# Kernel tuning notes

Measured on AMD Instinct MI355X. Metric: run time of the kernel, lower is better.

Reference implementation:

```python
import jax, jax.numpy as jnp
import numpy as np

N, E, IN, C, H = 50000, 1600000, 128, 64, 2
HC = H * C  # 128; num_out = 128, conv_out channels per head = 64
NEG_SLOPE = 0.2


def setup_inputs() -> dict:
    key = jax.random.key(0)
    ks = jax.random.split(key, 16)
    x = jax.random.normal(ks[0], (N, IN), dtype=jnp.float32)
    edge_index = jax.random.randint(ks[1], (2, E), 0, N, dtype=jnp.int64)

    def gat_params(k, fan_in, heads, out_ch):
        k1, k2, k3 = jax.random.split(k, 3)
        sc = 1.0 / np.sqrt(fan_in)
        W = jax.random.normal(k1, (fan_in, heads * out_ch), dtype=jnp.float32) * sc
        a_src = jax.random.normal(k2, (heads, out_ch), dtype=jnp.float32) * 0.1
        a_dst = jax.random.normal(k3, (heads, out_ch), dtype=jnp.float32) * 0.1
        b = jnp.zeros((heads * out_ch,), dtype=jnp.float32)
        return W, a_src, a_dst, b

    W_in, a_src_in, a_dst_in, b_in = gat_params(ks[2], IN, H, C)
    # 2 hidden layers, stacked on leading axis
    Wh, ash, adh, bh = [], [], [], []
    for i in range(2):
        W, a_s, a_d, b = gat_params(ks[3 + i], HC, H, C)
        Wh.append(W); ash.append(a_s); adh.append(a_d); bh.append(b)
    W_h = jnp.stack(Wh); a_src_h = jnp.stack(ash)
    a_dst_h = jnp.stack(adh); b_h = jnp.stack(bh)
    W_out, a_src_out, a_dst_out, b_out = gat_params(ks[6], HC, H, C)
    return dict(x=x, edge_index=edge_index,
                W_in=W_in, a_src_in=a_src_in, a_dst_in=a_dst_in, b_in=b_in,
                W_h=W_h, a_src_h=a_src_h, a_dst_h=a_dst_h, b_h=b_h,
                W_out=W_out, a_src_out=a_src_out, a_dst_out=a_dst_out, b_out=b_out)


def gat_layer(xf, src, dst, W, a_src, a_dst, b, heads, out_ch):
    n = xf.shape[0]
    h = (xf @ W).reshape(n, heads, out_ch)              # [N,H,C]
    e_src = jnp.einsum('nhc,hc->nh', h, a_src)          # [N,H]
    e_dst = jnp.einsum('nhc,hc->nh', h, a_dst)
    e = jax.nn.leaky_relu(e_src[src] + e_dst[dst], NEG_SLOPE)  # [E',H]
    m = jax.ops.segment_max(e, dst, num_segments=n)     # softmax over edges per dst
    p = jnp.exp(e - m[dst])
    s = jax.ops.segment_sum(p, dst, num_segments=n)
    alpha = p / (s[dst] + 1e-16)
    out = jax.ops.segment_sum(alpha[:, :, None] * h[src], dst, num_segments=n)
    return out.reshape(n, heads * out_ch) + b


def reference(x, edge_index, W_in, a_src_in, a_dst_in, b_in,
              W_h, a_src_h, a_dst_h, b_h,
              W_out, a_src_out, a_dst_out, b_out):
    # add self loops (PyG GATConv default add_self_loops=True)
    loops = jnp.arange(N, dtype=edge_index.dtype)
    src = jnp.concatenate([edge_index[0], loops])
    dst = jnp.concatenate([edge_index[1], loops])

    h = jax.nn.relu(gat_layer(x, src, dst, W_in, a_src_in, a_dst_in, b_in, H, C))
    for i in range(2):
        h = jax.nn.relu(gat_layer(h, src, dst, W_h[i], a_src_h[i], a_dst_h[i], b_h[i], H, C))
    out = gat_layer(h, src, dst, W_out, a_src_out, a_dst_out, b_out, H, C)
    return out
```

## Files before the change

### kernel.cpp

```cpp
#include <hip/hip_runtime.h>

#define NNODES 50000
#define NEDGES 1600000
#define NEG_SLOPE 0.2f

#define SCAN_NB 256
#define SCAN_CH 196

#define MT_ROWS 64
#define NMT 782
#define GEMM_BLOCKS 768

typedef __attribute__((ext_vector_type(8))) short short8;
typedef __attribute__((ext_vector_type(4))) float f32x4;
typedef __attribute__((ext_vector_type(4))) unsigned short us4;

static __device__ __forceinline__ unsigned short f2bf(float f) {
    unsigned u = __float_as_uint(f);
    unsigned r = u + 0x7FFFu + ((u >> 16) & 1u);
    return (unsigned short)(r >> 16);
}
static __device__ __forceinline__ float bf2f(unsigned short h) {
    return __uint_as_float(((unsigned)h) << 16);
}
static __device__ __forceinline__ unsigned short f2h(float f) {
    union { _Float16 x; unsigned short u; } c;
    c.x = (_Float16)f;
    return c.u;
}
static __device__ __forceinline__ float h2f(unsigned short u) {
    union { unsigned short u; _Float16 x; } c;
    c.u = u;
    return (float)c.x;
}


__global__ void k_count(const int* __restrict__ ei, int* __restrict__ count,
                        int* __restrict__ pos) {
    int t = blockIdx.x * blockDim.x + threadIdx.x;
    int stride = gridDim.x * blockDim.x;
    #pragma unroll
    for (int i = 0; i < 8; i++) {
        int e = t + i * stride;
        if (e < NEDGES) pos[e] = atomicAdd(&count[ei[NEDGES + e]], 1);
    }
}

__global__ __launch_bounds__(256) void k_bsum(const int* __restrict__ count,
                                              int* __restrict__ bsum) {
    __shared__ int red[4];
    int t = threadIdx.x, b = blockIdx.x;
    int idx = b * SCAN_CH + t;
    int v = (t < SCAN_CH && idx < NNODES) ? count[idx] + 1 : 0;
    #pragma unroll
    for (int m = 1; m <= 32; m <<= 1) v += __shfl_xor(v, m);
    if ((t & 63) == 0) red[t >> 6] = v;
    __syncthreads();
    if (t == 0) bsum[b] = red[0] + red[1] + red[2] + red[3];
}

__global__ __launch_bounds__(256) void k_bscan(const int* __restrict__ bsum,
                                               int* __restrict__ boff,
                                               int* __restrict__ row_ptr) {
    __shared__ int s[256];
    int t = threadIdx.x;
    int v = bsum[t];
    s[t] = v;
    __syncthreads();
    for (int off = 1; off < 256; off <<= 1) {
        int u = (t >= off) ? s[t - off] : 0;
        __syncthreads();
        s[t] += u;
        __syncthreads();
    }
    boff[t] = s[t] - v;
    if (t == 255) row_ptr[NNODES] = s[255];
}

__global__ __launch_bounds__(256) void k_rowptr(const int* __restrict__ count,
                                                const int* __restrict__ boff,
                                                int* __restrict__ row_ptr,
                                                int* __restrict__ csr_src) {
    __shared__ int s[256];
    int t = threadIdx.x, b = blockIdx.x;
    int idx = b * SCAN_CH + t;
    bool valid = (t < SCAN_CH && idx < NNODES);
    int v = valid ? count[idx] + 1 : 0;
    s[t] = v;
    __syncthreads();
    for (int off = 1; off < 256; off <<= 1) {
        int u = (t >= off) ? s[t - off] : 0;
        __syncthreads();
        s[t] += u;
        __syncthreads();
    }
    if (valid) {
        int run = boff[b] + s[t] - v;
        row_ptr[idx] = run;
        csr_src[run] = idx;
    }
}

__global__ void k_scatter(const int* __restrict__ ei, const int* __restrict__ row_ptr,
                          const int* __restrict__ pos, int* __restrict__ csr_src) {
    int t = blockIdx.x * blockDim.x + threadIdx.x;
    int stride = gridDim.x * blockDim.x;
    #pragma unroll
    for (int i = 0; i < 4; i++) {
        int e = t + i * stride;
        if (e < NEDGES) {
            int s = ei[e];
            int d = ei[NEDGES + e];
            __builtin_nontemporal_store(s, &csr_src[row_ptr[d] + 1 + pos[e]]);
        }
    }
}

__global__ __launch_bounds__(256) void k_wprep(const float* __restrict__ W0,
                                               const float* __restrict__ Wh,
                                               const float* __restrict__ Wout,
                                               unsigned short* __restrict__ wthi,
                                               unsigned short* __restrict__ wtlo) {
    int t = blockIdx.x * blockDim.x + threadIdx.x;
    int l = t >> 14;
    int i = t & 16383;
    int k = i >> 7, n = i & 127;
    const float* src = (l == 0) ? W0 : (l == 3) ? Wout : (Wh + (size_t)(l - 1) * 16384);
    float v = src[i];
    unsigned short h = f2bf(v);
    wthi[(size_t)l * 16384 + n * 128 + k] = h;
    wtlo[(size_t)l * 16384 + n * 128 + k] = f2bf(v - bf2f(h));
}

__global__ __launch_bounds__(256, 3) void k_gemm_mfma(
        const float* __restrict__ X,
        const unsigned short* __restrict__ Ahi, const unsigned short* __restrict__ Alo,
        const unsigned short* __restrict__ Wthi, const unsigned short* __restrict__ Wtlo,
        const float* __restrict__ a_src, const float* __restrict__ a_dst,
        unsigned short* __restrict__ Hh,
        float* __restrict__ e_src, float* __restrict__ e_dst, int use_x)
{
    __shared__ __align__(16) short sAhi[MT_ROWS * 128];
    __shared__ __align__(16) short sAlo[MT_ROWS * 128];
    __shared__ float eS[4][MT_ROWS];
    __shared__ float eD[4][MT_ROWS];

    const int tid  = threadIdx.x;
    const int lane = tid & 63;
    const int w    = tid >> 6;
    const int l15  = lane & 15;
    const int quad = lane >> 4;

    short8 Bh[2][4], Bl[2][4];
    #pragma unroll
    for (int nt = 0; nt < 2; nt++) {
        int n = w * 32 + nt * 16 + l15;
        #pragma unroll
        for (int ks = 0; ks < 4; ks++) {
            Bh[nt][ks] = *(const short8*)(Wthi + (size_t)n * 128 + ks * 32 + quad * 8);
            Bl[nt][ks] = *(const short8*)(Wtlo + (size_t)n * 128 + ks * 32 + quad * 8);
        }
    }
    float as0 = a_src[w * 32 + l15],      ad0 = a_dst[w * 32 + l15];
    float as1 = a_src[w * 32 + 16 + l15], ad1 = a_dst[w * 32 + 16 + l15];

    for (int mt0 = blockIdx.x; mt0 < NMT; mt0 += GEMM_BLOCKS) {
        const int row0 = mt0 * MT_ROWS;

        for (int i = tid; i < MT_ROWS * 16; i += 256) {
            int m  = i >> 4;
            int kc = i & 15;
            int g  = row0 + m; if (g > NNODES - 1) g = NNODES - 1;
            int cp = kc ^ (m & 15);
            short8 vh, vl;
            if (use_x) {
                float4 xa = *(const float4*)(X + (size_t)g * 128 + kc * 8);
                float4 xb = *(const float4*)(X + (size_t)g * 128 + kc * 8 + 4);
                float xs[8] = {xa.x, xa.y, xa.z, xa.w, xb.x, xb.y, xb.z, xb.w};
                #pragma unroll
                for (int q = 0; q < 8; q++) {
                    unsigned short h = f2bf(xs[q]);
                    vh[q] = (short)h;
                    vl[q] = (short)f2bf(xs[q] - bf2f(h));
                }
            } else {
                vh = *(const short8*)(Ahi + (size_t)g * 128 + kc * 8);
                vl = *(const short8*)(Alo + (size_t)g * 128 + kc * 8);
            }
            *(short8*)&sAhi[m * 128 + cp * 8] = vh;
            *(short8*)&sAlo[m * 128 + cp * 8] = vl;
        }
        __syncthreads();

        f32x4 zero = {0.f, 0.f, 0.f, 0.f};
        f32x4 acc[4][2];
        #pragma unroll
        for (int mt = 0; mt < 4; mt++) { acc[mt][0] = zero; acc[mt][1] = zero; }
        #pragma unroll
        for (int mt = 0; mt < 4; mt++) {
            int m = mt * 16 + l15;
            #pragma unroll
            for (int ks = 0; ks < 4; ks++) {
                int kc = ks * 4 + quad;
                int cp = kc ^ l15;
                short8 ah = *(const short8*)&sAhi[m * 128 + cp * 8];
                short8 al = *(const short8*)&sAlo[m * 128 + cp * 8];
                #pragma unroll
                for (int nt = 0; nt < 2; nt++) {
                    acc[mt][nt] = __builtin_amdgcn_mfma_f32_16x16x32_bf16(ah, Bh[nt][ks], acc[mt][nt], 0, 0, 0);
                    acc[mt][nt] = __builtin_amdgcn_mfma_f32_16x16x32_bf16(al, Bh[nt][ks], acc[mt][nt], 0, 0, 0);
                    acc[mt][nt] = __builtin_amdgcn_mfma_f32_16x16x32_bf16(ah, Bl[nt][ks], acc[mt][nt], 0, 0, 0);
                }
            }
        }

        #pragma unroll
        for (int mt = 0; mt < 4; mt++) {
            #pragma unroll
            for (int r = 0; r < 4; r++) {
                int m = mt * 16 + quad * 4 + r;
                int g = row0 + m;
                float v0 = acc[mt][0][r], v1 = acc[mt][1][r];
                if (g < NNODES) {
                    int n0 = w * 32 + l15;
                    Hh[(size_t)g * 128 + n0]      = f2h(v0);
                    Hh[(size_t)g * 128 + n0 + 16] = f2h(v1);
                }
                float ps = v0 * as0 + v1 * as1;
                float pd = v0 * ad0 + v1 * ad1;
                ps += __shfl_xor(ps, 1); ps += __shfl_xor(ps, 2);
                ps += __shfl_xor(ps, 4); ps += __shfl_xor(ps, 8);
                pd += __shfl_xor(pd, 1); pd += __shfl_xor(pd, 2);
                pd += __shfl_xor(pd, 4); pd += __shfl_xor(pd, 8);
                if (l15 == 0) { eS[w][m] = ps; eD[w][m] = pd; }
            }
        }
        __syncthreads();
        if (tid < MT_ROWS * 2) {
            int m = tid >> 1, head = tid & 1;
            int g = row0 + m;
            if (g < NNODES) {
                e_src[g * 2 + head] = eS[head * 2][m] + eS[head * 2 + 1][m];
                e_dst[g * 2 + head] = eD[head * 2][m] + eD[head * 2 + 1][m];
            }
        }
        __syncthreads();
    }
}

__global__ __launch_bounds__(256) void k_aggregate_h(const unsigned short* __restrict__ Hh,
                                                     const float* __restrict__ e_src,
                                                     const float* __restrict__ e_dst,
                                                     const int* __restrict__ row_ptr,
                                                     const int* __restrict__ csr_src,
                                                     const float* __restrict__ bias,
                                                     unsigned short* __restrict__ ohi,
                                                     unsigned short* __restrict__ olo) {
    int lane = threadIdx.x & 63;
    int wv   = threadIdx.x >> 6;
    int d    = blockIdx.x * 4 + wv;
    if (d >= NNODES) return;
    int half = lane >> 5;
    int li   = lane & 31;
    int head = li >> 4;
    int c0   = li * 4;
    float ed = e_dst[d * 2 + head];
    int beg = row_ptr[d], end = row_ptr[d + 1];
    f32x4 acc = {0.f, 0.f, 0.f, 0.f};
    float ssum = 0.f;
    int j = beg;
    for (; j + 16 <= end; j += 16) {
        int s[8];
        #pragma unroll
        for (int u = 0; u < 8; u++) s[u] = csr_src[j + 2 * u + half];
        us4 q[8];
        #pragma unroll
        for (int u = 0; u < 8; u++) q[u] = *(const us4*)(Hh + (size_t)s[u] * 128 + c0);
        float p[8];
        #pragma unroll
        for (int u = 0; u < 8; u++) {
            float t = e_src[s[u] * 2 + head] + ed;
            t = t > 0.f ? t : NEG_SLOPE * t;
            p[u] = __expf(t);
        }
        #pragma unroll
        for (int u = 0; u < 8; u++) {
            acc[0] += p[u] * h2f(q[u][0]);
            acc[1] += p[u] * h2f(q[u][1]);
            acc[2] += p[u] * h2f(q[u][2]);
            acc[3] += p[u] * h2f(q[u][3]);
            ssum   += p[u];
        }
    }
    for (; j < end; j += 2) {
        int idx = j + half;
        bool valid = idx < end;
        int s = csr_src[valid ? idx : end - 1];
        float t = e_src[s * 2 + head] + ed;
        t = t > 0.f ? t : NEG_SLOPE * t;
        float p = valid ? __expf(t) : 0.f;
        us4 q = *(const us4*)(Hh + (size_t)s * 128 + c0);
        acc[0] += p * h2f(q[0]);
        acc[1] += p * h2f(q[1]);
        acc[2] += p * h2f(q[2]);
        acc[3] += p * h2f(q[3]);
        ssum   += p;
    }
    acc[0] += __shfl_xor(acc[0], 32);
    acc[1] += __shfl_xor(acc[1], 32);
    acc[2] += __shfl_xor(acc[2], 32);
    acc[3] += __shfl_xor(acc[3], 32);
    ssum   += __shfl_xor(ssum,   32);
    if (half == 0) {
        float inv = 1.0f / ssum;
        float4 bv = *(const float4*)(bias + c0);
        float o0 = fmaxf(acc[0] * inv + bv.x, 0.f);
        float o1 = fmaxf(acc[1] * inv + bv.y, 0.f);
        float o2 = fmaxf(acc[2] * inv + bv.z, 0.f);
        float o3 = fmaxf(acc[3] * inv + bv.w, 0.f);
        unsigned short h0 = f2bf(o0), h1 = f2bf(o1), h2 = f2bf(o2), h3 = f2bf(o3);
        *(ushort4*)&ohi[(size_t)d * 128 + c0] = make_ushort4(h0, h1, h2, h3);
        *(ushort4*)&olo[(size_t)d * 128 + c0] =
            make_ushort4(f2bf(o0 - bf2f(h0)), f2bf(o1 - bf2f(h1)),
                         f2bf(o2 - bf2f(h2)), f2bf(o3 - bf2f(h3)));
    }
}

__global__ __launch_bounds__(256) void k_aggregate_f(const unsigned short* __restrict__ Hh,
                                                     const float* __restrict__ e_src,
                                                     const float* __restrict__ e_dst,
                                                     const int* __restrict__ row_ptr,
                                                     const int* __restrict__ csr_src,
                                                     const float* __restrict__ bias,
                                                     float* __restrict__ outf) {
    int lane = threadIdx.x & 63;
    int wv   = threadIdx.x >> 6;
    int d    = blockIdx.x * 4 + wv;
    if (d >= NNODES) return;
    int half = lane >> 5;
    int li   = lane & 31;
    int head = li >> 4;
    int c0   = li * 4;
    float ed = e_dst[d * 2 + head];
    int beg = row_ptr[d], end = row_ptr[d + 1];
    f32x4 acc = {0.f, 0.f, 0.f, 0.f};
    float ssum = 0.f;
    int j = beg;
    for (; j + 16 <= end; j += 16) {
        int s[8];
        #pragma unroll
        for (int u = 0; u < 8; u++) s[u] = csr_src[j + 2 * u + half];
        us4 q[8];
        #pragma unroll
        for (int u = 0; u < 8; u++) q[u] = *(const us4*)(Hh + (size_t)s[u] * 128 + c0);
        float p[8];
        #pragma unroll
        for (int u = 0; u < 8; u++) {
            float t = e_src[s[u] * 2 + head] + ed;
            t = t > 0.f ? t : NEG_SLOPE * t;
            p[u] = __expf(t);
        }
        #pragma unroll
        for (int u = 0; u < 8; u++) {
            acc[0] += p[u] * h2f(q[u][0]);
            acc[1] += p[u] * h2f(q[u][1]);
            acc[2] += p[u] * h2f(q[u][2]);
            acc[3] += p[u] * h2f(q[u][3]);
            ssum   += p[u];
        }
    }
    for (; j < end; j += 2) {
        int idx = j + half;
        bool valid = idx < end;
        int s = csr_src[valid ? idx : end - 1];
        float t = e_src[s * 2 + head] + ed;
        t = t > 0.f ? t : NEG_SLOPE * t;
        float p = valid ? __expf(t) : 0.f;
        us4 q = *(const us4*)(Hh + (size_t)s * 128 + c0);
        acc[0] += p * h2f(q[0]);
        acc[1] += p * h2f(q[1]);
        acc[2] += p * h2f(q[2]);
        acc[3] += p * h2f(q[3]);
        ssum   += p;
    }
    acc[0] += __shfl_xor(acc[0], 32);
    acc[1] += __shfl_xor(acc[1], 32);
    acc[2] += __shfl_xor(acc[2], 32);
    acc[3] += __shfl_xor(acc[3], 32);
    ssum   += __shfl_xor(ssum,   32);
    if (half == 0) {
        float inv = 1.0f / ssum;
        float4 bv = *(const float4*)(bias + c0);
        *(float4*)(outf + (size_t)d * 128 + c0) =
            make_float4(acc[0] * inv + bv.x, acc[1] * inv + bv.y,
                        acc[2] * inv + bv.z, acc[3] * inv + bv.w);
    }
}


extern "C" void kernel_launch(void* const* d_in, const int* in_sizes, int n_in,
                              void* d_out, int out_size, void* d_ws, size_t ws_size,
                              hipStream_t stream) {
    const float* x  = (const float*)d_in[0];
    const int*   ei = (const int*)d_in[1];

    char* ws = (char*)d_ws;
    size_t off = 0;
    auto alloc = [&](size_t bytes) {
        void* p = ws + off;
        off = (off + bytes + 255) & ~(size_t)255;
        return p;
    };
    int*            count   = (int*)alloc((size_t)NNODES * 4);
    int*            row_ptr = (int*)alloc((size_t)(NNODES + 1) * 4);
    int*            csr     = (int*)alloc((size_t)(NEDGES + NNODES) * 4);
    int*            pos     = (int*)alloc((size_t)NEDGES * 4);
    int*            bsum    = (int*)alloc((size_t)SCAN_NB * 4);
    int*            boff    = (int*)alloc((size_t)SCAN_NB * 4);
    unsigned short* hh      = (unsigned short*)alloc((size_t)NNODES * 128 * 2);
    unsigned short* wthi    = (unsigned short*)alloc((size_t)4 * 16384 * 2);
    unsigned short* wtlo    = (unsigned short*)alloc((size_t)4 * 16384 * 2);
    float*          es      = (float*)alloc((size_t)NNODES * 2 * 4);
    float*          edv     = (float*)alloc((size_t)NNODES * 2 * 4);
    (void)ws_size; (void)in_sizes; (void)n_in; (void)out_size;

    unsigned short* hi = (unsigned short*)d_out;
    unsigned short* lo = hi + (size_t)NNODES * 128;

    const float* W0   = (const float*)d_in[2];
    const float* W_h  = (const float*)d_in[6];
    const float* Wout = (const float*)d_in[10];

    hipMemsetAsync(count, 0, (size_t)NNODES * 4, stream);
    k_count  <<<(NEDGES + 8 * 256 - 1) / (8 * 256), 256, 0, stream>>>(ei, count, pos);
    k_wprep  <<<256, 256, 0, stream>>>(W0, W_h, Wout, wthi, wtlo);
    k_bsum   <<<SCAN_NB, 256, 0, stream>>>(count, bsum);
    k_bscan  <<<1, 256, 0, stream>>>(bsum, boff, row_ptr);
    k_rowptr <<<SCAN_NB, 256, 0, stream>>>(count, boff, row_ptr, csr);
    k_scatter<<<(NEDGES + 4 * 256 - 1) / (4 * 256), 256, 0, stream>>>(ei, row_ptr, pos, csr);

    const float* ash = (const float*)d_in[7];
    const float* adh = (const float*)d_in[8];
    const float* bh  = (const float*)d_in[9];

    struct Layer { const float *as, *ad, *b; };
    Layer L[4] = {
        { (const float*)d_in[3],  (const float*)d_in[4],  (const float*)d_in[5]  },
        { ash,        adh,        bh        },
        { ash + 128,  adh + 128,  bh + 128  },
        { (const float*)d_in[11], (const float*)d_in[12], (const float*)d_in[13] },
    };

    const int agg_blocks = (NNODES + 3) / 4;
    for (int l = 0; l < 4; l++) {
        k_gemm_mfma<<<GEMM_BLOCKS, 256, 0, stream>>>(
            x, hi, lo, wthi + (size_t)l * 16384, wtlo + (size_t)l * 16384,
            L[l].as, L[l].ad, hh, es, edv, l == 0 ? 1 : 0);
        if (l < 3) {
            k_aggregate_h<<<agg_blocks, 256, 0, stream>>>(hh, es, edv, row_ptr, csr,
                                                          L[l].b, hi, lo);
        } else {
            k_aggregate_f<<<agg_blocks, 256, 0, stream>>>(hh, es, edv, row_ptr, csr,
                                                          L[l].b, (float*)d_out);
        }
    }
}
```

Before: 597.2 us.

## Fuse edge counting into first GEMM launch and widen aggregation gathers to 8 halves

Result: faster. 537.6 us (-10.0%).

```diff
diff --git a/kernel.cpp b/kernel.cpp
--- a/kernel.cpp
+++ b/kernel.cpp
@@ -10,10 +10,12 @@
 #define MT_ROWS 64
 #define NMT 782
 #define GEMM_BLOCKS 768
+#define COUNT_BLOCKS 256
 
 typedef __attribute__((ext_vector_type(8))) short short8;
 typedef __attribute__((ext_vector_type(4))) float f32x4;
-typedef __attribute__((ext_vector_type(4))) unsigned short us4;
+typedef __attribute__((ext_vector_type(8))) _Float16 h16x8;
+typedef __attribute__((ext_vector_type(8))) unsigned short us8;
 
 static __device__ __forceinline__ unsigned short f2bf(float f) {
     unsigned u = __float_as_uint(f);
@@ -28,23 +30,7 @@
     c.x = (_Float16)f;
     return c.u;
 }
-static __device__ __forceinline__ float h2f(unsigned short u) {
-    union { unsigned short u; _Float16 x; } c;
-    c.u = u;
-    return (float)c.x;
-}
-
-
-__global__ void k_count(const int* __restrict__ ei, int* __restrict__ count,
-                        int* __restrict__ pos) {
-    int t = blockIdx.x * blockDim.x + threadIdx.x;
-    int stride = gridDim.x * blockDim.x;
-    #pragma unroll
-    for (int i = 0; i < 8; i++) {
-        int e = t + i * stride;
-        if (e < NEDGES) pos[e] = atomicAdd(&count[ei[NEDGES + e]], 1);
-    }
-}
+
 
 __global__ __launch_bounds__(256) void k_bsum(const int* __restrict__ count,
                                               int* __restrict__ bsum) {
@@ -138,12 +124,25 @@
         const unsigned short* __restrict__ Wthi, const unsigned short* __restrict__ Wtlo,
         const float* __restrict__ a_src, const float* __restrict__ a_dst,
         unsigned short* __restrict__ Hh,
-        float* __restrict__ e_src, float* __restrict__ e_dst, int use_x)
+        float* __restrict__ e_src, float* __restrict__ e_dst, int use_x,
+        const int* __restrict__ ei, int* __restrict__ count, int* __restrict__ pos)
 {
     __shared__ __align__(16) short sAhi[MT_ROWS * 128];
     __shared__ __align__(16) short sAlo[MT_ROWS * 128];
     __shared__ float eS[4][MT_ROWS];
     __shared__ float eD[4][MT_ROWS];
+
+    if (blockIdx.x >= GEMM_BLOCKS) {
+        int t = (blockIdx.x - GEMM_BLOCKS) * 256 + threadIdx.x;
+        for (int base = t; base < NEDGES; base += 8 * 65536) {
+            #pragma unroll
+            for (int i = 0; i < 8; i++) {
+                int e = base + i * 65536;
+                if (e < NEDGES) pos[e] = atomicAdd(&count[ei[NEDGES + e]], 1);
+            }
+        }
+        return;
+    }
 
     const int tid  = threadIdx.x;
     const int lane = tid & 63;
@@ -248,6 +247,96 @@
     }
 }
 
+template <int FINAL>
+__device__ __forceinline__ void agg_body(const _Float16* __restrict__ Hh,
+                                         const float* __restrict__ e_src,
+                                         const float* __restrict__ e_dst,
+                                         const int* __restrict__ row_ptr,
+                                         const int* __restrict__ csr_src,
+                                         const float* __restrict__ bias,
+                                         float* __restrict__ outf,
+                                         unsigned short* __restrict__ ohi,
+                                         unsigned short* __restrict__ olo) {
+    int lane = threadIdx.x & 63;
+    int wv   = threadIdx.x >> 6;
+    int d    = blockIdx.x * 4 + wv;
+    if (d >= NNODES) return;
+    int qt   = lane >> 4;
+    int cl   = lane & 15;
+    int head = cl >> 3;
+    int c0   = cl * 8;
+    float ed = e_dst[d * 2 + head];
+    int beg = row_ptr[d], end = row_ptr[d + 1];
+    float acc[8] = {0.f, 0.f, 0.f, 0.f, 0.f, 0.f, 0.f, 0.f};
+    float ssum = 0.f;
+    int j = beg;
+    for (; j + 16 <= end; j += 16) {
+        int s0 = csr_src[j + qt],      s1 = csr_src[j + 4 + qt];
+        int s2 = csr_src[j + 8 + qt],  s3 = csr_src[j + 12 + qt];
+        h16x8 h0 = *(const h16x8*)(Hh + (size_t)s0 * 128 + c0);
+        h16x8 h1 = *(const h16x8*)(Hh + (size_t)s1 * 128 + c0);
+        h16x8 h2 = *(const h16x8*)(Hh + (size_t)s2 * 128 + c0);
+        h16x8 h3 = *(const h16x8*)(Hh + (size_t)s3 * 128 + c0);
+        float t0 = e_src[s0 * 2 + head] + ed, t1 = e_src[s1 * 2 + head] + ed;
+        float t2 = e_src[s2 * 2 + head] + ed, t3 = e_src[s3 * 2 + head] + ed;
+        t0 = t0 > 0.f ? t0 : NEG_SLOPE * t0;  t1 = t1 > 0.f ? t1 : NEG_SLOPE * t1;
+        t2 = t2 > 0.f ? t2 : NEG_SLOPE * t2;  t3 = t3 > 0.f ? t3 : NEG_SLOPE * t3;
+        float p0 = __expf(t0), p1 = __expf(t1), p2 = __expf(t2), p3 = __expf(t3);
+        #pragma unroll
+        for (int c = 0; c < 8; c++)
+            acc[c] += p0 * (float)h0[c] + p1 * (float)h1[c]
+                    + p2 * (float)h2[c] + p3 * (float)h3[c];
+        ssum += p0 + p1 + p2 + p3;
+    }
+    for (; j < end; j += 4) {
+        int idx = j + qt;
+        bool valid = idx < end;
+        int s = csr_src[valid ? idx : end - 1];
+        float t = e_src[s * 2 + head] + ed;
+        t = t > 0.f ? t : NEG_SLOPE * t;
+        float p = valid ? __expf(t) : 0.f;
+        h16x8 hq = *(const h16x8*)(Hh + (size_t)s * 128 + c0);
+        #pragma unroll
+        for (int c = 0; c < 8; c++) acc[c] += p * (float)hq[c];
+        ssum += p;
+    }
+    #pragma unroll
+    for (int c = 0; c < 8; c++) {
+        acc[c] += __shfl_xor(acc[c], 16);
+        acc[c] += __shfl_xor(acc[c], 32);
+    }
+    ssum += __shfl_xor(ssum, 16);
+    ssum += __shfl_xor(ssum, 32);
+    if (qt == 0) {
+        float inv = 1.0f / ssum;
+        f32x4 b0 = *(const f32x4*)(bias + c0);
+        f32x4 b1 = *(const f32x4*)(bias + c0 + 4);
+        float o[8];
+        #pragma unroll
+        for (int c = 0; c < 8; c++) {
+            float bv = (c < 4) ? b0[c] : b1[c - 4];
+            o[c] = acc[c] * inv + bv;
+        }
+        if (FINAL) {
+            f32x4 w0 = {o[0], o[1], o[2], o[3]};
+            f32x4 w1 = {o[4], o[5], o[6], o[7]};
+            *(f32x4*)(outf + (size_t)d * 128 + c0)     = w0;
+            *(f32x4*)(outf + (size_t)d * 128 + c0 + 4) = w1;
+        } else {
+            us8 vh, vl;
+            #pragma unroll
+            for (int c = 0; c < 8; c++) {
+                float oc = fmaxf(o[c], 0.f);
+                unsigned short hbits = f2bf(oc);
+                vh[c] = hbits;
+                vl[c] = f2bf(oc - bf2f(hbits));
+            }
+            *(us8*)&ohi[(size_t)d * 128 + c0] = vh;
+            *(us8*)&olo[(size_t)d * 128 + c0] = vl;
+        }
+    }
+}
+
 __global__ __launch_bounds__(256) void k_aggregate_h(const unsigned short* __restrict__ Hh,
                                                      const float* __restrict__ e_src,
                                                      const float* __restrict__ e_dst,
@@ -256,74 +345,8 @@
                                                      const float* __restrict__ bias,
                                                      unsigned short* __restrict__ ohi,
                                                      unsigned short* __restrict__ olo) {
-    int lane = threadIdx.x & 63;
-    int wv   = threadIdx.x >> 6;
-    int d    = blockIdx.x * 4 + wv;
-    if (d >= NNODES) return;
-    int half = lane >> 5;
-    int li   = lane & 31;
-    int head = li >> 4;
-    int c0   = li * 4;
-    float ed = e_dst[d * 2 + head];
-    int beg = row_ptr[d], end = row_ptr[d + 1];
-    f32x4 acc = {0.f, 0.f, 0.f, 0.f};
-    float ssum = 0.f;
-    int j = beg;
-    for (; j + 16 <= end; j += 16) {
-        int s[8];
-        #pragma unroll
-        for (int u = 0; u < 8; u++) s[u] = csr_src[j + 2 * u + half];
-        us4 q[8];
-        #pragma unroll
-        for (int u = 0; u < 8; u++) q[u] = *(const us4*)(Hh + (size_t)s[u] * 128 + c0);
-        float p[8];
-        #pragma unroll
-        for (int u = 0; u < 8; u++) {
-            float t = e_src[s[u] * 2 + head] + ed;
-            t = t > 0.f ? t : NEG_SLOPE * t;
-            p[u] = __expf(t);
-        }
-        #pragma unroll
-        for (int u = 0; u < 8; u++) {
-            acc[0] += p[u] * h2f(q[u][0]);
-            acc[1] += p[u] * h2f(q[u][1]);
-            acc[2] += p[u] * h2f(q[u][2]);
-            acc[3] += p[u] * h2f(q[u][3]);
-            ssum   += p[u];
-        }
-    }
-    for (; j < end; j += 2) {
-        int idx = j + half;
-        bool valid = idx < end;
-        int s = csr_src[valid ? idx : end - 1];
-        float t = e_src[s * 2 + head] + ed;
-        t = t > 0.f ? t : NEG_SLOPE * t;
-        float p = valid ? __expf(t) : 0.f;
-        us4 q = *(const us4*)(Hh + (size_t)s * 128 + c0);
-        acc[0] += p * h2f(q[0]);
-        acc[1] += p * h2f(q[1]);
-        acc[2] += p * h2f(q[2]);
-        acc[3] += p * h2f(q[3]);
-        ssum   += p;
-    }
-    acc[0] += __shfl_xor(acc[0], 32);
-    acc[1] += __shfl_xor(acc[1], 32);
-    acc[2] += __shfl_xor(acc[2], 32);
-    acc[3] += __shfl_xor(acc[3], 32);
-    ssum   += __shfl_xor(ssum,   32);
-    if (half == 0) {
-        float inv = 1.0f / ssum;
-        float4 bv = *(const float4*)(bias + c0);
-        float o0 = fmaxf(acc[0] * inv + bv.x, 0.f);
-        float o1 = fmaxf(acc[1] * inv + bv.y, 0.f);
-        float o2 = fmaxf(acc[2] * inv + bv.z, 0.f);
-        float o3 = fmaxf(acc[3] * inv + bv.w, 0.f);
-        unsigned short h0 = f2bf(o0), h1 = f2bf(o1), h2 = f2bf(o2), h3 = f2bf(o3);
-        *(ushort4*)&ohi[(size_t)d * 128 + c0] = make_ushort4(h0, h1, h2, h3);
-        *(ushort4*)&olo[(size_t)d * 128 + c0] =
-            make_ushort4(f2bf(o0 - bf2f(h0)), f2bf(o1 - bf2f(h1)),
-                         f2bf(o2 - bf2f(h2)), f2bf(o3 - bf2f(h3)));
-    }
+    agg_body<0>((const _Float16*)Hh, e_src, e_dst, row_ptr, csr_src, bias,
+                nullptr, ohi, olo);
 }
 
 __global__ __launch_bounds__(256) void k_aggregate_f(const unsigned short* __restrict__ Hh,
@@ -333,68 +356,8 @@
                                                      const int* __restrict__ csr_src,
                                                      const float* __restrict__ bias,
                                                      float* __restrict__ outf) {
-    int lane = threadIdx.x & 63;
-    int wv   = threadIdx.x >> 6;
-    int d    = blockIdx.x * 4 + wv;
-    if (d >= NNODES) return;
-    int half = lane >> 5;
-    int li   = lane & 31;
-    int head = li >> 4;
-    int c0   = li * 4;
-    float ed = e_dst[d * 2 + head];
-    int beg = row_ptr[d], end = row_ptr[d + 1];
-    f32x4 acc = {0.f, 0.f, 0.f, 0.f};
-    float ssum = 0.f;
-    int j = beg;
-    for (; j + 16 <= end; j += 16) {
-        int s[8];
-        #pragma unroll
-        for (int u = 0; u < 8; u++) s[u] = csr_src[j + 2 * u + half];
-        us4 q[8];
-        #pragma unroll
-        for (int u = 0; u < 8; u++) q[u] = *(const us4*)(Hh + (size_t)s[u] * 128 + c0);
-        float p[8];
-        #pragma unroll
-        for (int u = 0; u < 8; u++) {
-            float t = e_src[s[u] * 2 + head] + ed;
-            t = t > 0.f ? t : NEG_SLOPE * t;
-            p[u] = __expf(t);
-        }
-        #pragma unroll
-        for (int u = 0; u < 8; u++) {
-            acc[0] += p[u] * h2f(q[u][0]);
-            acc[1] += p[u] * h2f(q[u][1]);
-            acc[2] += p[u] * h2f(q[u][2]);
-            acc[3] += p[u] * h2f(q[u][3]);
-            ssum   += p[u];
-        }
-    }
-    for (; j < end; j += 2) {
-        int idx = j + half;
-        bool valid = idx < end;
-        int s = csr_src[valid ? idx : end - 1];
-        float t = e_src[s * 2 + head] + ed;
-        t = t > 0.f ? t : NEG_SLOPE * t;
-        float p = valid ? __expf(t) : 0.f;
-        us4 q = *(const us4*)(Hh + (size_t)s * 128 + c0);
-        acc[0] += p * h2f(q[0]);
-        acc[1] += p * h2f(q[1]);
-        acc[2] += p * h2f(q[2]);
-        acc[3] += p * h2f(q[3]);
-        ssum   += p;
-    }
-    acc[0] += __shfl_xor(acc[0], 32);
-    acc[1] += __shfl_xor(acc[1], 32);
-    acc[2] += __shfl_xor(acc[2], 32);
-    acc[3] += __shfl_xor(acc[3], 32);
-    ssum   += __shfl_xor(ssum,   32);
-    if (half == 0) {
-        float inv = 1.0f / ssum;
-        float4 bv = *(const float4*)(bias + c0);
-        *(float4*)(outf + (size_t)d * 128 + c0) =
-            make_float4(acc[0] * inv + bv.x, acc[1] * inv + bv.y,
-                        acc[2] * inv + bv.z, acc[3] * inv + bv.w);
-    }
+    agg_body<1>((const _Float16*)Hh, e_src, e_dst, row_ptr, csr_src, bias,
+                outf, nullptr, nullptr);
 }
 
 
@@ -431,14 +394,6 @@
     const float* W_h  = (const float*)d_in[6];
     const float* Wout = (const float*)d_in[10];
 
-    hipMemsetAsync(count, 0, (size_t)NNODES * 4, stream);
-    k_count  <<<(NEDGES + 8 * 256 - 1) / (8 * 256), 256, 0, stream>>>(ei, count, pos);
-    k_wprep  <<<256, 256, 0, stream>>>(W0, W_h, Wout, wthi, wtlo);
-    k_bsum   <<<SCAN_NB, 256, 0, stream>>>(count, bsum);
-    k_bscan  <<<1, 256, 0, stream>>>(bsum, boff, row_ptr);
-    k_rowptr <<<SCAN_NB, 256, 0, stream>>>(count, boff, row_ptr, csr);
-    k_scatter<<<(NEDGES + 4 * 256 - 1) / (4 * 256), 256, 0, stream>>>(ei, row_ptr, pos, csr);
-
     const float* ash = (const float*)d_in[7];
     const float* adh = (const float*)d_in[8];
     const float* bh  = (const float*)d_in[9];
@@ -451,11 +406,21 @@
         { (const float*)d_in[11], (const float*)d_in[12], (const float*)d_in[13] },
     };
 
+    hipMemsetAsync(count, 0, (size_t)NNODES * 4, stream);
+    k_wprep<<<256, 256, 0, stream>>>(W0, W_h, Wout, wthi, wtlo);
+
     const int agg_blocks = (NNODES + 3) / 4;
     for (int l = 0; l < 4; l++) {
-        k_gemm_mfma<<<GEMM_BLOCKS, 256, 0, stream>>>(
+        int grid = (l == 0) ? GEMM_BLOCKS + COUNT_BLOCKS : GEMM_BLOCKS;
+        k_gemm_mfma<<<grid, 256, 0, stream>>>(
             x, hi, lo, wthi + (size_t)l * 16384, wtlo + (size_t)l * 16384,
-            L[l].as, L[l].ad, hh, es, edv, l == 0 ? 1 : 0);
+            L[l].as, L[l].ad, hh, es, edv, l == 0 ? 1 : 0, ei, count, pos);
+        if (l == 0) {
+            k_bsum   <<<SCAN_NB, 256, 0, stream>>>(count, bsum);
+            k_bscan  <<<1, 256, 0, stream>>>(bsum, boff, row_ptr);
+            k_rowptr <<<SCAN_NB, 256, 0, stream>>>(count, boff, row_ptr, csr);
+            k_scatter<<<(NEDGES + 4 * 256 - 1) / (4 * 256), 256, 0, stream>>>(ei, row_ptr, pos, csr);
+        }
         if (l < 3) {
             k_aggregate_h<<<agg_blocks, 256, 0, stream>>>(hh, es, edv, row_ptr, csr,
                                                           L[l].b, hi, lo);
```
